# Kernel tuning notes

Hardware: AMD Instinct MI355X
Metric: run time of the kernel (lower is better)

## Reference

```python
import jax, jax.numpy as jnp
import numpy as np

B, S, D = 4, 2048, 1024
H, DK, DV = 16, 64, 64


def setup_inputs() -> dict:
    key = jax.random.key(0)
    ks = jax.random.split(key, 12)
    sd = 0.02
    return {
        "input_query": jax.random.normal(ks[0], (B, S, D), jnp.float32),
        "input_key": jax.random.normal(ks[1], (B, S, D), jnp.float32),
        "input_value": jax.random.normal(ks[2], (B, S, D), jnp.float32),
        "Wq": jax.random.normal(ks[3], (H, D, DK), jnp.float32) * sd,
        "bq": jax.random.normal(ks[4], (H, DK), jnp.float32) * sd,
        "Wk": jax.random.normal(ks[5], (H, D, DK), jnp.float32) * sd,
        "bk": jax.random.normal(ks[6], (H, DK), jnp.float32) * sd,
        "Wv": jax.random.normal(ks[7], (H, D, DV), jnp.float32) * sd,
        "bv": jax.random.normal(ks[8], (H, DV), jnp.float32) * sd,
        "Wo": jax.random.normal(ks[9], (H * DV, D), jnp.float32) * sd,
        "bo": jax.random.normal(ks[10], (D,), jnp.float32) * sd,
    }


def reference(input_query, input_key, input_value, Wq, bq, Wk, bk, Wv, bv, Wo, bo):
    # per-head projections, batched over all heads at once
    q = jnp.einsum("bsd,hdk->bhsk", input_query, Wq) + bq[None, :, None, :]
    k = jnp.einsum("bsd,hdk->bhsk", input_key, Wk) + bk[None, :, None, :]
    v = jnp.einsum("bsd,hdv->bhsv", input_value, Wv) + bv[None, :, None, :]
    # NOTE: original code computes self.dk = sqrt(d_k) but never divides by it,
    # so scores are UNSCALED QK^T (faithful to the source).
    score = jnp.einsum("bhqk,bhsk->bhqs", q, k)  # [B,H,S,S]
    score = jax.nn.softmax(score, axis=-1)
    z = jnp.einsum("bhqs,bhsv->bhqv", score, v)  # [B,H,S,DV]
    # concat heads along feature dim (dim=2 in torch) -> [B,S,H*DV]
    z = jnp.transpose(z, (0, 2, 1, 3)).reshape(z.shape[0], z.shape[2], -1)
    return z @ Wo + bo
```

## Files before the change

### kernel.cpp

```cpp
#include <hip/hip_runtime.h>


using short8  = __attribute__((ext_vector_type(8))) short;
using short4_t= __attribute__((ext_vector_type(4))) short;
using floatx4 = __attribute__((ext_vector_type(4))) float;

#define MFMA32(a, b, c) __builtin_amdgcn_mfma_f32_16x16x32_bf16((a), (b), (c), 0, 0, 0)
#define MFMA16(a, b, c) __builtin_amdgcn_mfma_f32_16x16x16bf16_1k((a), (b), (c), 0, 0, 0)

__device__ __forceinline__ void async16(const unsigned short* g, unsigned short* lds_base) {
  __builtin_amdgcn_global_load_lds(
      (const __attribute__((address_space(1))) unsigned int*)g,
      (__attribute__((address_space(3))) unsigned int*)lds_base, 16, 0, 0);
}

__device__ __forceinline__ float bf2f(unsigned short u) {
  union { unsigned int i; float f; } v; v.i = ((unsigned int)u) << 16; return v.f;
}
__device__ __forceinline__ unsigned short f2bf(float f) {
  union { float f; unsigned int i; } v; v.f = f;
  unsigned int r = v.i + 0x7FFFu + ((v.i >> 16) & 1u);
  return (unsigned short)(r >> 16);
}
__device__ __forceinline__ unsigned int fbits(float f) {
  union { float f; unsigned int i; } v; v.f = f; return v.i;
}
__device__ __forceinline__ unsigned short ld_bf(const void* p, size_t idx, int isbf16) {
  return isbf16 ? ((const unsigned short*)p)[idx] : f2bf(((const float*)p)[idx]);
}
__device__ __forceinline__ float ld_f(const void* p, size_t idx, int isbf16) {
  return isbf16 ? bf2f(((const unsigned short*)p)[idx]) : ((const float*)p)[idx];
}

__global__ void detect_dtype(const unsigned int* __restrict__ X,
                             unsigned int* __restrict__ flag) {
  __shared__ int red[256];
  int cnt = 0;
  for (int i = threadIdx.x; i < 4096; i += 256) {
    unsigned int e = (X[i] >> 7) & 0xFFu;
    cnt += (e >= 96u && e <= 160u) ? 1 : 0;
  }
  red[threadIdx.x] = cnt;
  __syncthreads();
  for (int s = 128; s > 0; s >>= 1) {
    if (threadIdx.x < (unsigned)s) red[threadIdx.x] += red[threadIdx.x + s];
    __syncthreads();
  }
  if (threadIdx.x == 0) *flag = (red[0] >= 2560) ? 1u : 0u;
}

__global__ __launch_bounds__(256) void prep(
    const void* __restrict__ Xq, const void* __restrict__ Xk,
    const void* __restrict__ Xv,
    const void* __restrict__ Wq, const void* __restrict__ Wk,
    const void* __restrict__ Wv, const void* __restrict__ Wo,
    unsigned short* __restrict__ Xqc, unsigned short* __restrict__ Xkc,
    unsigned short* __restrict__ Xvc,
    unsigned short* __restrict__ WT,
    unsigned short* __restrict__ WoT,
    const unsigned int* __restrict__ flagp)
{
  const int isbf16 = (int)*flagp;
  const int bid = blockIdx.x, tid = threadIdx.x;

  if (bid < 12288) {
    const int z = bid >> 12;
    const int i = ((bid & 4095) << 8) + tid;
    const void* X = (z == 0) ? Xq : (z == 1) ? Xk : Xv;
    unsigned short* Y = (z == 0) ? Xqc : (z == 1) ? Xkc : Xvc;
    if (isbf16) {
      ((uint4*)Y)[i] = ((const uint4*)X)[i];
    } else {
      const float* f = (const float*)X + (size_t)i * 8;
      union { unsigned short u[8]; uint4 v; } t;
#pragma unroll
      for (int j = 0; j < 8; ++j) t.u[j] = f2bf(f[j]);
      ((uint4*)Y)[i] = t.v;
    }
    return;
  }

  __shared__ unsigned short tile[32][33];
  const int tx = tid & 31, ty = tid >> 5;
  const int t = bid - 12288;
  if (t < 3072) {
    const int x = t & 1, y = (t >> 1) & 31, zz = t >> 6;
    const int w = zz >> 4, hh = zz & 15;
    const void* in = (w == 0) ? Wq : (w == 1) ? Wk : Wv;
    const size_t boff = (size_t)hh * 1024 * 64;
    unsigned short* op = WT + ((size_t)w << 20) + boff;
    const int r0 = y * 32, c0 = x * 32;
#pragma unroll
    for (int i = 0; i < 4; ++i) {
      int r = ty + i * 8;
      tile[r][tx] = ld_bf(in, boff + (size_t)(r0 + r) * 64 + (c0 + tx), isbf16);
    }
    __syncthreads();
#pragma unroll
    for (int i = 0; i < 4; ++i) {
      int c = ty + i * 8;
      op[(size_t)(c0 + c) * 1024 + (r0 + tx)] = tile[tx][c];
    }
  } else {
    const int t2 = t - 3072;
    const int x = t2 & 31, y = t2 >> 5;
    const int r0 = y * 32, c0 = x * 32;
#pragma unroll
    for (int i = 0; i < 4; ++i) {
      int r = ty + i * 8;
      tile[r][tx] = ld_bf(Wo, (size_t)(r0 + r) * 1024 + (c0 + tx), isbf16);
    }
    __syncthreads();
#pragma unroll
    for (int i = 0; i < 4; ++i) {
      int c = ty + i * 8;
      WoT[(size_t)(c0 + c) * 1024 + (r0 + tx)] = tile[tx][c];
    }
  }
}

#define GEMM_MAIN_LOOP(Aq, Btq, Kdim)                                          \
  floatx4 acc[4][4];                                                           \
  _Pragma("unroll") for (int i = 0; i < 4; ++i)                                \
      _Pragma("unroll") for (int j = 0; j < 4; ++j)                            \
          acc[i][j] = (floatx4){0.f, 0.f, 0.f, 0.f};                           \
  const int lrow = lane >> 3, cg = lane & 7;                                   \
  const int scol = ((cg ^ lrow) * 8);                                          \
  const int sw = ln15 & 7;                                                     \
  for (int k0 = 0; k0 < (Kdim); k0 += 64) {                                    \
    __syncthreads();                                                           \
    _Pragma("unroll") for (int r = 0; r < 4; ++r) {                            \
      const int chunk = r * 4 + wave;                                          \
      const int row = chunk * 8 + lrow;                                        \
      async16(&(Aq)[(size_t)(m0 + row) * (Kdim) + k0 + scol],                  \
              &a_lds[(size_t)chunk * 512]);                                    \
      async16(&(Btq)[(size_t)(n0 + row) * (Kdim) + k0 + scol],                 \
              &b_lds[(size_t)chunk * 512]);                                    \
    }                                                                          \
    __syncthreads();                                                           \
    _Pragma("unroll") for (int kk = 0; kk < 2; ++kk) {                         \
      short8 af[4];                                                            \
      _Pragma("unroll") for (int i = 0; i < 4; ++i)                            \
          af[i] = *(const short8*)&a_lds[(wm + i * 16 + ln15) * 64 +           \
                                         (((kk * 4 + quad) ^ sw) * 8)];        \
      _Pragma("unroll") for (int j = 0; j < 4; ++j) {                          \
        short8 bf = *(const short8*)&b_lds[(wn + j * 16 + ln15) * 64 +         \
                                           (((kk * 4 + quad) ^ sw) * 8)];      \
        _Pragma("unroll") for (int i = 0; i < 4; ++i)                          \
            acc[i][j] = MFMA32(af[i], bf, acc[i][j]);                          \
      }                                                                        \
    }                                                                          \
  }

__global__ __launch_bounds__(256) void gemm_qkv(
    const unsigned short* __restrict__ A0, const unsigned short* __restrict__ A1,
    const unsigned short* __restrict__ A2,
    const unsigned short* __restrict__ BT,
    const void* __restrict__ b0, const void* __restrict__ b1,
    const void* __restrict__ b2,
    unsigned short* __restrict__ Qp, unsigned short* __restrict__ Kp,
    unsigned short* __restrict__ Vt,
    const unsigned int* __restrict__ flagp)
{
  const int isbf16 = (int)*flagp;
  const int z = blockIdx.z;
  const unsigned short* A  = (z == 0) ? A0 : (z == 1) ? A1 : A2;
  const unsigned short* Bt = BT + ((size_t)z << 20);
  const void* bias = (z == 0) ? b0 : (z == 1) ? b1 : b2;
  const int m0 = blockIdx.x * 128, n0 = blockIdx.y * 128;
  const int tid = threadIdx.x, wave = tid >> 6, lane = tid & 63;
  const int ln15 = lane & 15, quad = lane >> 4;
  const int wm = (wave >> 1) * 64, wn = (wave & 1) * 64;
  __shared__ alignas(16) unsigned short a_lds[128 * 64];
  __shared__ alignas(16) unsigned short b_lds[128 * 64];

  GEMM_MAIN_LOOP(A, Bt, 1024)

  if (z < 2) {
    unsigned short* C = z ? Kp : Qp;
#pragma unroll
    for (int j = 0; j < 4; ++j) {
      const int col = n0 + wn + j * 16 + ln15;
      const float bv = ld_f(bias, col, isbf16);
#pragma unroll
      for (int i = 0; i < 4; ++i) {
        const int row = m0 + wm + i * 16 + quad * 4;
#pragma unroll
        for (int r = 0; r < 4; ++r)
          C[(size_t)(row + r) * 1024 + col] = f2bf(acc[i][j][r] + bv);
      }
    }
  } else {
    __syncthreads();
#pragma unroll
    for (int j = 0; j < 4; ++j) {
      const int nl = wn + j * 16 + ln15;
      const float bv = ld_f(bias, n0 + nl, isbf16);
      unsigned short* dst = (nl < 64) ? &a_lds[(size_t)nl * 128]
                                      : &b_lds[(size_t)(nl - 64) * 128];
#pragma unroll
      for (int i = 0; i < 4; ++i) {
        const int ml = wm + i * 16 + quad * 4;
#pragma unroll
        for (int r = 0; r < 4; ++r) dst[ml + r] = f2bf(acc[i][j][r] + bv);
      }
    }
    __syncthreads();
    const int nl = tid >> 1, half = tid & 1;
    const unsigned short* src = (nl < 64) ? &a_lds[(size_t)nl * 128 + half * 64]
                                          : &b_lds[(size_t)(nl - 64) * 128 + half * 64];
    const int bb = m0 >> 11, s0 = m0 & 2047;
    unsigned short* dst = Vt + (size_t)bb * 2048 * 1024 +
                          (size_t)(n0 + nl) * 2048 + s0 + half * 64;
#pragma unroll
    for (int c = 0; c < 8; ++c) *(uint4*)&dst[c * 8] = *(const uint4*)&src[c * 8];
  }
}

__global__ __launch_bounds__(256) void gemm_out(
    const unsigned short* __restrict__ A,
    const unsigned short* __restrict__ Bt,
    const void* __restrict__ bias,
    void* __restrict__ C,
    const unsigned int* __restrict__ flagp)
{
  const int isbf16 = (int)*flagp;
  const int m0 = blockIdx.x * 128, n0 = blockIdx.y * 128;
  const int tid = threadIdx.x, wave = tid >> 6, lane = tid & 63;
  const int ln15 = lane & 15, quad = lane >> 4;
  const int wm = (wave >> 1) * 64, wn = (wave & 1) * 64;
  __shared__ alignas(16) unsigned short a_lds[128 * 64];
  __shared__ alignas(16) unsigned short b_lds[128 * 64];

  GEMM_MAIN_LOOP(A, Bt, 1024)

#pragma unroll
  for (int j = 0; j < 4; ++j) {
    const int col = n0 + wn + j * 16 + ln15;
    const float bv = ld_f(bias, col, isbf16);
#pragma unroll
    for (int i = 0; i < 4; ++i) {
      const int row = m0 + wm + i * 16 + quad * 4;
#pragma unroll
      for (int r = 0; r < 4; ++r) {
        const float val = acc[i][j][r] + bv;
        if (!isbf16) ((float*)C)[(size_t)(row + r) * 1024 + col] = val;
        else ((unsigned short*)C)[(size_t)(row + r) * 1024 + col] = f2bf(val);
      }
    }
  }
}

__global__ __launch_bounds__(256, 2) void attn(
    const unsigned short* __restrict__ Q,
    const unsigned short* __restrict__ K,
    const unsigned short* __restrict__ Vt,
    unsigned short* __restrict__ Z)
{
  const int qt0 = blockIdx.x * 256, h = blockIdx.y, b = blockIdx.z;
  const int tid = threadIdx.x, wave = tid >> 6, lane = tid & 63;
  const int ln15 = lane & 15, quad = lane >> 4;

  __shared__ alignas(16) char smem[55296];
  unsigned short* q_lds = (unsigned short*)smem;
  unsigned short* k_lds = (unsigned short*)(smem + 36864);
  unsigned short* v_lds = (unsigned short*)(smem + 46080);

  const unsigned short* Qb = Q + ((size_t)(b * 2048 + qt0)) * 1024 + h * 64;
  const unsigned short* Kb = K + ((size_t)(b * 2048)) * 1024 + h * 64;
  const unsigned short* Vh = Vt + (size_t)b * 2048 * 1024 + (size_t)h * 64 * 2048;

  const int sr = tid >> 2, sc = (tid & 3) * 16;
#pragma unroll
  for (int i = 0; i < 4; ++i) {
    const int r = sr + i * 64;
    *(uint4*)&q_lds[r * 72 + sc]     = *(const uint4*)&Qb[(size_t)r * 1024 + sc];
    *(uint4*)&q_lds[r * 72 + sc + 8] = *(const uint4*)&Qb[(size_t)r * 1024 + sc + 8];
  }
  __syncthreads();
  short8 qf[4][2];
#pragma unroll
  for (int g = 0; g < 4; ++g) {
    const int row = (g * 4 + wave) * 16 + ln15;
    qf[g][0] = *(const short8*)&q_lds[row * 72 + quad * 8];
    qf[g][1] = *(const short8*)&q_lds[row * 72 + 32 + quad * 8];
  }

  floatx4 o_acc[4][4];
#pragma unroll
  for (int g = 0; g < 4; ++g)
#pragma unroll
    for (int vb = 0; vb < 4; ++vb) o_acc[g][vb] = (floatx4){0.f, 0.f, 0.f, 0.f};
  float l_part[4] = {0.f, 0.f, 0.f, 0.f};

  for (int j0 = 0; j0 < 2048; j0 += 64) {
    __syncthreads();
    *(uint4*)&k_lds[sr * 72 + sc]     = *(const uint4*)&Kb[(size_t)(j0 + sr) * 1024 + sc];
    *(uint4*)&k_lds[sr * 72 + sc + 8] = *(const uint4*)&Kb[(size_t)(j0 + sr) * 1024 + sc + 8];
    *(uint4*)&v_lds[sr * 72 + sc]     = *(const uint4*)&Vh[(size_t)sr * 2048 + j0 + sc];
    *(uint4*)&v_lds[sr * 72 + sc + 8] = *(const uint4*)&Vh[(size_t)sr * 2048 + j0 + sc + 8];
    __syncthreads();

    short8 kf[4][2];
    short4_t vf[4][4];
#pragma unroll
    for (int nb = 0; nb < 4; ++nb) {
      kf[nb][0] = *(const short8*)&k_lds[(nb * 16 + ln15) * 72 + quad * 8];
      kf[nb][1] = *(const short8*)&k_lds[(nb * 16 + ln15) * 72 + 32 + quad * 8];
    }
#pragma unroll
    for (int vb = 0; vb < 4; ++vb)
#pragma unroll
      for (int nb = 0; nb < 4; ++nb)
        vf[vb][nb] = *(const short4_t*)&v_lds[(vb * 16 + ln15) * 72 + nb * 16 + quad * 4];

#pragma unroll
    for (int g = 0; g < 4; ++g) {
      short4_t pb[4];
#pragma unroll
      for (int nb = 0; nb < 4; ++nb) {
        floatx4 st = (floatx4){0.f, 0.f, 0.f, 0.f};
        st = MFMA32(kf[nb][0], qf[g][0], st);
        st = MFMA32(kf[nb][1], qf[g][1], st);
        const float p0 = __expf(st[0]), p1 = __expf(st[1]);
        const float p2 = __expf(st[2]), p3 = __expf(st[3]);
        l_part[g] += (p0 + p1) + (p2 + p3);
        union { unsigned int u[2]; short4_t s; } pk;
        pk.u[0] = (fbits(p0) >> 16) | (fbits(p1) & 0xFFFF0000u);
        pk.u[1] = (fbits(p2) >> 16) | (fbits(p3) & 0xFFFF0000u);
        pb[nb] = pk.s;
      }
#pragma unroll
      for (int vb = 0; vb < 4; ++vb)
#pragma unroll
        for (int nb = 0; nb < 4; ++nb)
          o_acc[g][vb] = MFMA16(vf[vb][nb], pb[nb], o_acc[g][vb]);
    }
  }

  __syncthreads();
  float* ot = (float*)smem;
  const int q = tid >> 2, vg = (tid & 3) * 16;
#pragma unroll
  for (int g = 0; g < 4; ++g) {
    float l = l_part[g];
    l += __shfl_xor(l, 16);
    l += __shfl_xor(l, 32);
    const float rl = 1.0f / l;
#pragma unroll
    for (int vb = 0; vb < 4; ++vb)
#pragma unroll
      for (int r = 0; r < 4; ++r)
        ot[(wave * 16 + ln15) * 66 + vb * 16 + quad * 4 + r] = o_acc[g][vb][r] * rl;
    __syncthreads();
    union { unsigned short u[16]; uint4 v[2]; } t;
#pragma unroll
    for (int i = 0; i < 16; ++i) t.u[i] = f2bf(ot[q * 66 + vg + i]);
    unsigned short* dst = Z + ((size_t)(b * 2048 + qt0 + g * 64 + q)) * 1024 + h * 64 + vg;
    *(uint4*)&dst[0] = t.v[0];
    *(uint4*)&dst[8] = t.v[1];
    __syncthreads();
  }
}

extern "C" void kernel_launch(void* const* d_in, const int* in_sizes, int n_in,
                              void* d_out, int out_size, void* d_ws, size_t ws_size,
                              hipStream_t stream) {
  const void* Xq = d_in[0];
  const void* Xk = d_in[1];
  const void* Xv = d_in[2];
  const void* Wq = d_in[3];
  const void* bq = d_in[4];
  const void* Wk = d_in[5];
  const void* bk = d_in[6];
  const void* Wv = d_in[7];
  const void* bv = d_in[8];
  const void* Wo = d_in[9];
  const void* bo = d_in[10];

  unsigned int*   flag = (unsigned int*)d_ws;
  unsigned short* base = (unsigned short*)d_ws + 128;
  unsigned short* WqT = base;
  unsigned short* WoT = WqT + (3u << 20);
  unsigned short* buf0 = WoT + (1u << 20);
  unsigned short* buf1 = buf0 + (8u << 20);
  unsigned short* buf2 = buf1 + (8u << 20);
  unsigned short* buf3 = buf2 + (8u << 20);
  unsigned short* buf4 = buf3 + (8u << 20);
  unsigned short* buf5 = buf4 + (8u << 20);
  unsigned short *Xqc = buf0, *Xkc = buf1, *Xvc = buf2;
  unsigned short *Qp = buf3, *Kp = buf4, *VtR = buf5;
  unsigned short *Zp = buf2;

  detect_dtype<<<1, 256, 0, stream>>>((const unsigned int*)Xq, flag);

  prep<<<16384, 256, 0, stream>>>(Xq, Xk, Xv, Wq, Wk, Wv, Wo,
                                  Xqc, Xkc, Xvc, WqT, WoT, flag);

  gemm_qkv<<<dim3(64, 8, 3), 256, 0, stream>>>(Xqc, Xkc, Xvc, WqT, bq, bk, bv,
                                               Qp, Kp, VtR, flag);

  attn<<<dim3(8, 16, 4), 256, 0, stream>>>(Qp, Kp, VtR, Zp);

  gemm_out<<<dim3(64, 8), 256, 0, stream>>>(Zp, WoT, bo, d_out, flag);
}
```

Measured before the change: 348.4 us.

## Double-buffer K/V tiles in attention and compute row sums via MFMA

The attention kernel now double-buffers K/V tiles in LDS, issuing loads for the next tile before computing the current one, so only one barrier is needed per iteration. Q fragments are loaded straight from global memory, so the Q staging area in LDS goes away and LDS use drops. The softmax denominator is accumulated by an extra MFMA against a vector of ones, which replaces the scalar adds and the cross-lane shuffles. The loop order is swapped to nb-outer so K fragments are loaded per nb, bf16 packing uses v_perm, launch bounds are relaxed, and the grid is reordered so blocks with the same batch and q-tile run adjacently. Risks are higher register pressure, the extra MFMA work, and occupancy changes from dropping the min-blocks hint.

```diff
diff --git a/kernel.cpp b/kernel.cpp
--- a/kernel.cpp
+++ b/kernel.cpp
@@ -251,90 +251,95 @@
   }
 }
 
-__global__ __launch_bounds__(256, 2) void attn(
+__global__ __launch_bounds__(256) void attn(
     const unsigned short* __restrict__ Q,
     const unsigned short* __restrict__ K,
     const unsigned short* __restrict__ Vt,
     unsigned short* __restrict__ Z)
 {
-  const int qt0 = blockIdx.x * 256, h = blockIdx.y, b = blockIdx.z;
+  const int h = blockIdx.x, b = blockIdx.y, qt0 = blockIdx.z * 256;
   const int tid = threadIdx.x, wave = tid >> 6, lane = tid & 63;
   const int ln15 = lane & 15, quad = lane >> 4;
 
-  __shared__ alignas(16) char smem[55296];
-  unsigned short* q_lds = (unsigned short*)smem;
-  unsigned short* k_lds = (unsigned short*)(smem + 36864);
-  unsigned short* v_lds = (unsigned short*)(smem + 46080);
+  __shared__ alignas(16) char smem[36864];
+  unsigned short* kbuf0 = (unsigned short*)smem;
+  unsigned short* vbuf0 = (unsigned short*)(smem + 9216);
+  unsigned short* kbuf1 = (unsigned short*)(smem + 18432);
+  unsigned short* vbuf1 = (unsigned short*)(smem + 27648);
 
   const unsigned short* Qb = Q + ((size_t)(b * 2048 + qt0)) * 1024 + h * 64;
   const unsigned short* Kb = K + ((size_t)(b * 2048)) * 1024 + h * 64;
   const unsigned short* Vh = Vt + (size_t)b * 2048 * 1024 + (size_t)h * 64 * 2048;
 
-  const int sr = tid >> 2, sc = (tid & 3) * 16;
-#pragma unroll
-  for (int i = 0; i < 4; ++i) {
-    const int r = sr + i * 64;
-    *(uint4*)&q_lds[r * 72 + sc]     = *(const uint4*)&Qb[(size_t)r * 1024 + sc];
-    *(uint4*)&q_lds[r * 72 + sc + 8] = *(const uint4*)&Qb[(size_t)r * 1024 + sc + 8];
-  }
-  __syncthreads();
   short8 qf[4][2];
 #pragma unroll
   for (int g = 0; g < 4; ++g) {
     const int row = (g * 4 + wave) * 16 + ln15;
-    qf[g][0] = *(const short8*)&q_lds[row * 72 + quad * 8];
-    qf[g][1] = *(const short8*)&q_lds[row * 72 + 32 + quad * 8];
+    qf[g][0] = *(const short8*)&Qb[(size_t)row * 1024 + quad * 8];
+    qf[g][1] = *(const short8*)&Qb[(size_t)row * 1024 + 32 + quad * 8];
   }
 
   floatx4 o_acc[4][4];
-#pragma unroll
-  for (int g = 0; g < 4; ++g)
+  floatx4 l_acc[4];
+#pragma unroll
+  for (int g = 0; g < 4; ++g) {
+    l_acc[g] = (floatx4){0.f, 0.f, 0.f, 0.f};
 #pragma unroll
     for (int vb = 0; vb < 4; ++vb) o_acc[g][vb] = (floatx4){0.f, 0.f, 0.f, 0.f};
-  float l_part[4] = {0.f, 0.f, 0.f, 0.f};
-
-  for (int j0 = 0; j0 < 2048; j0 += 64) {
-    __syncthreads();
-    *(uint4*)&k_lds[sr * 72 + sc]     = *(const uint4*)&Kb[(size_t)(j0 + sr) * 1024 + sc];
-    *(uint4*)&k_lds[sr * 72 + sc + 8] = *(const uint4*)&Kb[(size_t)(j0 + sr) * 1024 + sc + 8];
-    *(uint4*)&v_lds[sr * 72 + sc]     = *(const uint4*)&Vh[(size_t)sr * 2048 + j0 + sc];
-    *(uint4*)&v_lds[sr * 72 + sc + 8] = *(const uint4*)&Vh[(size_t)sr * 2048 + j0 + sc + 8];
-    __syncthreads();
-
-    short8 kf[4][2];
+  }
+  const short4_t ones = {(short)0x3F80, (short)0x3F80, (short)0x3F80, (short)0x3F80};
+
+  const int sr = tid >> 2, sc = (tid & 3) * 16;
+  const unsigned short* Krow = &Kb[(size_t)sr * 1024];
+  const unsigned short* Vrow = &Vh[(size_t)sr * 2048];
+
+  {
+    *(uint4*)&kbuf0[sr * 72 + sc]     = *(const uint4*)&Krow[sc];
+    *(uint4*)&kbuf0[sr * 72 + sc + 8] = *(const uint4*)&Krow[sc + 8];
+    *(uint4*)&vbuf0[sr * 72 + sc]     = *(const uint4*)&Vrow[sc];
+    *(uint4*)&vbuf0[sr * 72 + sc + 8] = *(const uint4*)&Vrow[sc + 8];
+  }
+
+  for (int t = 0; t < 32; ++t) {
+    __syncthreads();
+    if (t < 31) {
+      const int j1 = (t + 1) * 64;
+      unsigned short* kn = (t & 1) ? kbuf0 : kbuf1;
+      unsigned short* vn = (t & 1) ? vbuf0 : vbuf1;
+      *(uint4*)&kn[sr * 72 + sc]     = *(const uint4*)&Krow[(size_t)j1 * 1024 + sc];
+      *(uint4*)&kn[sr * 72 + sc + 8] = *(const uint4*)&Krow[(size_t)j1 * 1024 + sc + 8];
+      *(uint4*)&vn[sr * 72 + sc]     = *(const uint4*)&Vrow[j1 + sc];
+      *(uint4*)&vn[sr * 72 + sc + 8] = *(const uint4*)&Vrow[j1 + sc + 8];
+    }
+    const unsigned short* kl = (t & 1) ? kbuf1 : kbuf0;
+    const unsigned short* vl = (t & 1) ? vbuf1 : vbuf0;
+
     short4_t vf[4][4];
 #pragma unroll
+    for (int vb = 0; vb < 4; ++vb)
+#pragma unroll
+      for (int nb = 0; nb < 4; ++nb)
+        vf[vb][nb] = *(const short4_t*)&vl[(vb * 16 + ln15) * 72 + nb * 16 + quad * 4];
+
+#pragma unroll
     for (int nb = 0; nb < 4; ++nb) {
-      kf[nb][0] = *(const short8*)&k_lds[(nb * 16 + ln15) * 72 + quad * 8];
-      kf[nb][1] = *(const short8*)&k_lds[(nb * 16 + ln15) * 72 + 32 + quad * 8];
-    }
-#pragma unroll
-    for (int vb = 0; vb < 4; ++vb)
-#pragma unroll
-      for (int nb = 0; nb < 4; ++nb)
-        vf[vb][nb] = *(const short4_t*)&v_lds[(vb * 16 + ln15) * 72 + nb * 16 + quad * 4];
-
-#pragma unroll
-    for (int g = 0; g < 4; ++g) {
-      short4_t pb[4];
-#pragma unroll
-      for (int nb = 0; nb < 4; ++nb) {
+      const short8 kf0 = *(const short8*)&kl[(nb * 16 + ln15) * 72 + quad * 8];
+      const short8 kf1 = *(const short8*)&kl[(nb * 16 + ln15) * 72 + 32 + quad * 8];
+#pragma unroll
+      for (int g = 0; g < 4; ++g) {
         floatx4 st = (floatx4){0.f, 0.f, 0.f, 0.f};
-        st = MFMA32(kf[nb][0], qf[g][0], st);
-        st = MFMA32(kf[nb][1], qf[g][1], st);
+        st = MFMA32(kf0, qf[g][0], st);
+        st = MFMA32(kf1, qf[g][1], st);
         const float p0 = __expf(st[0]), p1 = __expf(st[1]);
         const float p2 = __expf(st[2]), p3 = __expf(st[3]);
-        l_part[g] += (p0 + p1) + (p2 + p3);
         union { unsigned int u[2]; short4_t s; } pk;
-        pk.u[0] = (fbits(p0) >> 16) | (fbits(p1) & 0xFFFF0000u);
-        pk.u[1] = (fbits(p2) >> 16) | (fbits(p3) & 0xFFFF0000u);
-        pb[nb] = pk.s;
+        pk.u[0] = __builtin_amdgcn_perm(fbits(p1), fbits(p0), 0x07060302u);
+        pk.u[1] = __builtin_amdgcn_perm(fbits(p3), fbits(p2), 0x07060302u);
+        l_acc[g] = MFMA16(ones, pk.s, l_acc[g]);
+#pragma unroll
+        for (int vb = 0; vb < 4; ++vb)
+          o_acc[g][vb] = MFMA16(vf[vb][nb], pk.s, o_acc[g][vb]);
       }
-#pragma unroll
-      for (int vb = 0; vb < 4; ++vb)
-#pragma unroll
-        for (int nb = 0; nb < 4; ++nb)
-          o_acc[g][vb] = MFMA16(vf[vb][nb], pb[nb], o_acc[g][vb]);
     }
   }
 
@@ -343,10 +348,7 @@
   const int q = tid >> 2, vg = (tid & 3) * 16;
 #pragma unroll
   for (int g = 0; g < 4; ++g) {
-    float l = l_part[g];
-    l += __shfl_xor(l, 16);
-    l += __shfl_xor(l, 32);
-    const float rl = 1.0f / l;
+    const float rl = 1.0f / l_acc[g][0];
 #pragma unroll
     for (int vb = 0; vb < 4; ++vb)
 #pragma unroll
@@ -400,7 +402,7 @@
   gemm_qkv<<<dim3(64, 8, 3), 256, 0, stream>>>(Xqc, Xkc, Xvc, WqT, bq, bk, bv,
                                                Qp, Kp, VtR, flag);
 
-  attn<<<dim3(8, 16, 4), 256, 0, stream>>>(Qp, Kp, VtR, Zp);
+  attn<<<dim3(16, 4, 8), 256, 0, stream>>>(Qp, Kp, VtR, Zp);
 
   gemm_out<<<dim3(64, 8), 256, 0, stream>>>(Zp, WoT, bo, d_out, flag);
 }
```

Result: slower. 390.1 us (+12.0%).
